# Performance work log

Hardware: AMD Instinct MI355X
Metric: run time of the kernel (lower is better)

## Reference

```python
import jax, jax.numpy as jnp
import numpy as np

LSTM_SIZE = 64
NUM_OPS = 5
NUM_LAYERS = 7  # 2 warmup anchors + 5 sampled layers (layer_id 2..6)


def _lstm_cell(x, h, c, w_ih, w_hh, b_ih, b_hh):
    # torch LSTMCell gate order: i, f, g, o
    g = x @ w_ih.T + b_ih + h @ w_hh.T + b_hh  # [1, 4*64]
    i, f, gg, o = jnp.split(g, 4, axis=1)
    c2 = jax.nn.sigmoid(f) * c + jax.nn.sigmoid(i) * jnp.tanh(gg)
    h2 = jax.nn.sigmoid(o) * jnp.tanh(c2)
    return h2, c2


def _sampler(embed, w_ih, w_hh, b_ih, b_hh, w_soft, b_soft, b_soft_no_learn,
             w_attn1, w_attn2, v_attn, prev_c, prev_h, use_bias, key):
    keys = jax.random.split(key, 20)  # 5 layers * (2 index + 2 op) samples
    k = 0
    anchors, anchors_w1, arc_seq = [], [], []
    log_prob = jnp.float32(0.0)
    entropy = jnp.float32(0.0)
    inputs = embed[0][None, :]
    # warmup: two anchor slots (anchors are zeros, per original code)
    for _ in range(2):
        prev_h, prev_c = _lstm_cell(inputs, prev_h, prev_c, w_ih, w_hh, b_ih, b_hh)
        anchors.append(jnp.zeros((1, LSTM_SIZE), jnp.float32))
        anchors_w1.append(prev_h @ w_attn1.T)
    for layer_id in range(2, NUM_LAYERS):
        idxs, ops = [], []
        # sample 2 previous-layer indices via tiny attention
        for _ in range(2):
            prev_h, prev_c = _lstm_cell(inputs, prev_h, prev_c, w_ih, w_hh, b_ih, b_hh)
            query = jnp.concatenate(anchors_w1, axis=0)            # [layer_id, 64]
            q = jnp.tanh(query + prev_h @ w_attn2.T)               # broadcast [layer_id, 64]
            logits = (q @ v_attn.T).reshape(layer_id)              # [layer_id]
            logits = logits / 5.0 + 1.1 * jnp.tanh(logits)
            index = jax.random.categorical(keys[k], logits); k += 1
            logp = jax.nn.log_softmax(logits)
            log_prob = log_prob + (-logp[index])
            entropy = entropy + jax.lax.stop_gradient(-jnp.sum(logp * jnp.exp(logp)))
            idxs.append(index)
            A = jnp.concatenate(anchors, axis=0)                   # [layer_id, 64]
            inputs = A[index][None, :]
        # sample 2 ops
        for _ in range(2):
            prev_h, prev_c = _lstm_cell(inputs, prev_h, prev_c, w_ih, w_hh, b_ih, b_hh)
            logits = (prev_h @ w_soft.T + b_soft)                  # [1, 5]
            logits = 1.1 / 2.5 * jnp.tanh(logits / 5.0)
            if use_bias:
                logits = logits + b_soft_no_learn
            logits = logits[0]
            op_id = jax.random.categorical(keys[k], logits); k += 1
            logp = jax.nn.log_softmax(logits)
            log_prob = log_prob + (-logp[op_id])
            entropy = entropy + jax.lax.stop_gradient(-jnp.sum(logp * jnp.exp(logp)))
            ops.append(op_id)
            inputs = embed[op_id + 1][None, :]
        # extra step producing this layer's anchor
        prev_h, prev_c = _lstm_cell(inputs, prev_h, prev_c, w_ih, w_hh, b_ih, b_hh)
        anchors.append(prev_h)
        anchors_w1.append(prev_h @ w_attn1.T)
        inputs = embed[0][None, :]
        # arc layout per layer after in-place fixups: [idx1, op1, idx2, op2]
        arc_seq += [idxs[0], ops[0], idxs[1], ops[1]]
    arc = jnp.stack(arc_seq)
    return arc, entropy, log_prob, prev_c, prev_h


def setup_inputs() -> dict:
    key = jax.random.key(0)
    ks = jax.random.split(key, 9)
    u = lambda k, shape: jax.random.uniform(k, shape, jnp.float32, -0.1, 0.1)
    return {
        "embed": u(ks[0], (6, LSTM_SIZE)),
        "w_ih": u(ks[1], (4 * LSTM_SIZE, LSTM_SIZE)),
        "w_hh": u(ks[2], (4 * LSTM_SIZE, LSTM_SIZE)),
        "b_ih": u(ks[3], (4 * LSTM_SIZE,)),
        "b_hh": u(ks[4], (4 * LSTM_SIZE,)),
        "w_soft": u(ks[5], (NUM_OPS, LSTM_SIZE)),
        "b_soft": jnp.array([[10.0, 10.0, 0.0, 0.0, 0.0]], jnp.float32),
        "b_soft_no_learn": jnp.array([[0.25, 0.25, -0.25, -0.25, -0.25]], jnp.float32),
        "w_attn1": u(ks[6], (LSTM_SIZE, LSTM_SIZE)),
        "w_attn2": u(ks[7], (LSTM_SIZE, LSTM_SIZE)),
        "v_attn": u(ks[8], (1, LSTM_SIZE)),
        "seed": 0,
    }


def reference(embed, w_ih, w_hh, b_ih, b_hh, w_soft, b_soft, b_soft_no_learn,
              w_attn1, w_attn2, v_attn, seed):
    key = jax.random.key(seed)
    k1, k2 = jax.random.split(key)
    zc = jnp.zeros((1, LSTM_SIZE), jnp.float32)
    zh = jnp.zeros((1, LSTM_SIZE), jnp.float32)
    arc1, ent1, lp1, c, h = _sampler(embed, w_ih, w_hh, b_ih, b_hh, w_soft, b_soft,
                                     b_soft_no_learn, w_attn1, w_attn2, v_attn,
                                     zc, zh, True, k1)
    arc2, ent2, lp2, _, _ = _sampler(embed, w_ih, w_hh, b_ih, b_hh, w_soft, b_soft,
                                     b_soft_no_learn, w_attn1, w_attn2, v_attn,
                                     c, h, False, k2)
    return (arc1, arc2, lp1 + lp2, ent1 + ent2)
```

## Files before the change

kernel.cpp:

```cpp
#include <hip/hip_runtime.h>
#include <cstdint>

#ifndef FASTMATH
#define FASTMATH 1
#endif

#define NT 512

__device__ __forceinline__ uint32_t rotl32_(uint32_t v, int d) {
  return (v << d) | (v >> (32 - d));
}

__device__ __forceinline__ void tf2x32(uint32_t k0, uint32_t k1,
                                       uint32_t x0, uint32_t x1,
                                       uint32_t& o0, uint32_t& o1) {
  const uint32_t k2 = k0 ^ k1 ^ 0x1BD11BDAu;
  x0 += k0; x1 += k1;
#define TF4(a,b,c,d) \
  x0 += x1; x1 = rotl32_(x1,a); x1 ^= x0; \
  x0 += x1; x1 = rotl32_(x1,b); x1 ^= x0; \
  x0 += x1; x1 = rotl32_(x1,c); x1 ^= x0; \
  x0 += x1; x1 = rotl32_(x1,d); x1 ^= x0;
  TF4(13,15,26,6)
  x0 += k1; x1 += k2 + 1u;
  TF4(17,29,16,24)
  x0 += k2; x1 += k0 + 2u;
  TF4(13,15,26,6)
  x0 += k0; x1 += k1 + 3u;
  TF4(17,29,16,24)
  x0 += k1; x1 += k2 + 4u;
  TF4(13,15,26,6)
  x0 += k2; x1 += k0 + 5u;
#undef TF4
  o0 = x0; o1 = x1;
}

#if FASTMATH
__device__ __forceinline__ float tanh_(float x) {
  float e = __expf(2.0f * x);
  return 1.0f - __fdividef(2.0f, e + 1.0f);
}
__device__ __forceinline__ float sig_(float x) {
  return __fdividef(1.0f, 1.0f + __expf(-x));
}
#define log_ __logf
#define exp_ __expf
#else
__device__ __forceinline__ float tanh_(float x) { return tanhf(x); }
__device__ __forceinline__ float sig_(float x) { return 0.5f * tanhf(0.5f * x) + 0.5f; }
#define log_ logf
#define exp_ expf
#endif

template <int CTRL>
__device__ __forceinline__ float dppf(float x) {
  return __int_as_float(__builtin_amdgcn_update_dpp(
      0, __float_as_int(x), CTRL, 0xF, 0xF, true));
}
template <int CTRL>
__device__ __forceinline__ int dppi(int x) {
  return __builtin_amdgcn_update_dpp(0, x, CTRL, 0xF, 0xF, true);
}
constexpr int QP1 = 0xB1;
constexpr int QP2 = 0x4E;
constexpr int HM  = 0x141;

__global__ __launch_bounds__(NT, 1)
void nas_controller(const float* __restrict__ embed,
                    const float* __restrict__ w_ih,
                    const float* __restrict__ w_hh,
                    const float* __restrict__ b_ih,
                    const float* __restrict__ b_hh,
                    const float* __restrict__ w_soft,
                    const float* __restrict__ b_soft,
                    const float* __restrict__ b_soft_nl,
                    const float* __restrict__ w_attn1,
                    const float* __restrict__ w_attn2,
                    const float* __restrict__ v_attn,
                    const int* __restrict__ seedp,
                    float* __restrict__ out) {
  const int tid  = threadIdx.x;
  const int lane = tid & 63;
  const int wid  = tid >> 6;
  const int row  = tid >> 1;
  const int half = tid & 1;

  __shared__ __align__(16) float attn1L[64 * 68];
  __shared__ __align__(16) float attn2L[64 * 68];
  __shared__ __align__(16) float wsoftL[5 * 68 + 8];
  __shared__ __align__(16) float vaL[64];
  __shared__ __align__(16) float preQ[13 * 256];
  __shared__ __align__(16) float aw1sL[8 * 68];
  __shared__ __align__(16) float hw2L[64];
  __shared__ __align__(16) float hB[64];
  __shared__ float cs[64];
  __shared__ float gates[256];
  __shared__ float gL[320];
  __shared__ float bsoftL[8], bnlL[8];
  __shared__ int   seliL;

  float4 wi[8], wh[8];
  {
    const float4* a = reinterpret_cast<const float4*>(w_ih) + row * 16 + half * 8;
#pragma unroll
    for (int j = 0; j < 8; ++j) wi[j] = a[j];
    const float4* b = reinterpret_cast<const float4*>(w_hh) + row * 16 + half * 8;
#pragma unroll
    for (int j = 0; j < 8; ++j) wh[j] = b[j];
  }
  const float bsum = b_ih[row] + b_hh[row];

  for (int i4 = tid; i4 < 1024; i4 += NT) {
    int r = i4 >> 4, c4 = i4 & 15;
    reinterpret_cast<float4*>(attn1L)[r * 17 + c4] =
        reinterpret_cast<const float4*>(w_attn1)[i4];
    reinterpret_cast<float4*>(attn2L)[r * 17 + c4] =
        reinterpret_cast<const float4*>(w_attn2)[i4];
  }
  for (int i = tid; i < 340; i += NT) {
    int r = i / 68, c = i % 68;
    wsoftL[i] = (c < 64) ? w_soft[r * 64 + c] : 0.f;
  }
  if (tid < 64) { vaL[tid] = v_attn[tid]; hB[tid] = 0.f; cs[tid] = 0.f; }
  if (tid < 8) {
    bsoftL[tid] = (tid < 5) ? b_soft[tid] : 0.f;
    bnlL[tid]   = (tid < 5) ? b_soft_nl[tid] : 0.f;
  }
  preQ[6 * 256 + tid] = 0.f;

  if (tid < 320) {
    int s_ = (tid >= 160) ? 1 : 0;
    int rem = tid - s_ * 160;
    int k = rem >> 3, i = rem & 7;
    uint32_t a, b, ka, kb, o0, o1;
    tf2x32(0u, (uint32_t)seedp[0], 0u, (uint32_t)s_, a, b);
    tf2x32(a, b, 0u, (uint32_t)k, ka, kb);
    tf2x32(ka, kb, 0u, (uint32_t)i, o0, o1);
    uint32_t bits = o0 ^ o1;
    const float TINY = 1.1754943508222875e-38f;
    float uu = __uint_as_float((bits >> 9) | 0x3f800000u) - 1.0f;
    uu = uu * (1.0f - TINY) + TINY;
    uu = fmaxf(TINY, uu);
    gL[tid] = -log_(-log_(uu));
  }

#pragma unroll
  for (int e = 0; e < 6; ++e) {
    const float4* x4 = reinterpret_cast<const float4*>(embed + e * 64) + half * 8;
    float a0 = 0, a1 = 0, a2 = 0, a3 = 0;
#pragma unroll
    for (int j = 0; j < 8; ++j) {
      float4 x = x4[j], w = wi[j];
      a0 = fmaf(w.x, x.x, a0); a1 = fmaf(w.y, x.y, a1);
      a2 = fmaf(w.z, x.z, a2); a3 = fmaf(w.w, x.w, a3);
    }
    float acc = (a0 + a1) + (a2 + a3);
    acc += __shfl_xor(acc, 1);
    if (half == 0) preQ[e * 256 + row] = acc;
  }

  __syncthreads();

  const float4* hU = reinterpret_cast<const float4*>(hB);
  float lp = 0.f, ent = 0.f;
  int srcSlot = 0, sIdx = 0;

  auto lstm = [&]() {
    const float4* h4 = reinterpret_cast<const float4*>(hB) + half * 8;
    float a0 = 0, a1 = 0, a2 = 0, a3 = 0;
#pragma unroll
    for (int j = 0; j < 8; ++j) {
      float4 x = h4[j], w = wh[j];
      a0 = fmaf(w.x, x.x, a0); a1 = fmaf(w.y, x.y, a1);
      a2 = fmaf(w.z, x.z, a2); a3 = fmaf(w.w, x.w, a3);
    }
    float acc = (a0 + a1) + (a2 + a3);
    acc += __shfl_xor(acc, 1);
    if (half == 0) gates[row] = acc + preQ[srcSlot * 256 + row] + bsum;
    __syncthreads();
    if (tid < 64) {
      float gi = gates[tid], gf = gates[64 + tid];
      float gg = gates[128 + tid], go = gates[192 + tid];
      float c2 = sig_(gf) * cs[tid] + sig_(gi) * tanh_(gg);
      float h2 = sig_(go) * tanh_(c2);
      cs[tid] = c2; hB[tid] = h2;
    }
  };

  auto matvecAll = [&](const float* W, float* dst) {
    const int r8 = tid >> 3, q = tid & 7;
    const float4* w4 = reinterpret_cast<const float4*>(W + r8 * 68 + q * 8);
    float4 wa = w4[0], wb = w4[1];
    const float4* h4 = reinterpret_cast<const float4*>(hB) + q * 2;
    float4 ha = h4[0], hb = h4[1];
    float acc = fmaf(wa.x, ha.x, fmaf(wa.y, ha.y, fmaf(wa.z, ha.z, wa.w * ha.w)));
    acc += fmaf(wb.x, hb.x, fmaf(wb.y, hb.y, fmaf(wb.z, hb.z, wb.w * hb.w)));
    acc += __shfl_xor(acc, 1);
    acc += __shfl_xor(acc, 2);
    acc += __shfl_xor(acc, 4);
    if (q == 0) dst[r8] = acc;
  };

  auto anchorPre = [&](int slot) {
    const float4* h4 = reinterpret_cast<const float4*>(hB) + half * 8;
    float a0 = 0, a1 = 0, a2 = 0, a3 = 0;
#pragma unroll
    for (int j = 0; j < 8; ++j) {
      float4 x = h4[j], w = wi[j];
      a0 = fmaf(w.x, x.x, a0); a1 = fmaf(w.y, x.y, a1);
      a2 = fmaf(w.z, x.z, a2); a3 = fmaf(w.w, x.w, a3);
    }
    float acc = (a0 + a1) + (a2 + a3);
    acc += __shfl_xor(acc, 1);
    if (half == 0) preQ[slot * 256 + row] = acc;
  };

  auto doSample = [&](int n, int k, int mode, float raw, float* op) {
    float l;
    if (lane < n) {
      if (mode == 0) l = raw / 5.0f + 1.1f * tanh_(raw);
      else {
        l = (float)(1.1 / 2.5) * tanh_(raw / 5.0f);
        if (mode == 1) l += bnlL[lane];
      }
    } else l = -INFINITY;
    float g = (lane < n) ? gL[sIdx * 160 + k * 8 + lane] : 0.f;
    float v = (lane < n) ? (l + g) : -INFINITY;
    int bi = lane & 7;
    float lw = l;
#define ARGSTEP(C) { float ov = dppf<C>(v), ol = dppf<C>(lw); int oi = dppi<C>(bi); \
    bool tk = (ov > v) || (ov == v && oi < bi); if (tk) { v = ov; lw = ol; bi = oi; } }
    ARGSTEP(QP1) ARGSTEP(QP2) ARGSTEP(HM)
#undef ARGSTEP
    float mx = l;
    mx = fmaxf(mx, dppf<QP1>(mx)); mx = fmaxf(mx, dppf<QP2>(mx)); mx = fmaxf(mx, dppf<HM>(mx));
    float e = (lane < n) ? exp_(l - mx) : 0.f;
    float ss = e; ss += dppf<QP1>(ss); ss += dppf<QP2>(ss); ss += dppf<HM>(ss);
    float lse = log_(ss);
    float lpi = l - mx - lse;
    float ec = (lane < n) ? lpi * exp_(lpi) : 0.f;
    ec += dppf<QP1>(ec); ec += dppf<QP2>(ec); ec += dppf<HM>(ec);
    if (lane == 0) {
      lp  += -(lw - mx - lse);
      ent += -ec;
      seliL = bi;
      op[0] = (float)bi;
    }
  };

  for (int s = 0; s < 2; ++s) {
    sIdx = s;
    srcSlot = 0;
    for (int w = 0; w < 2; ++w) {
      lstm();
      __syncthreads();
      matvecAll(attn1L, aw1sL + w * 68);
    }
    int keyk = 0;
    for (int L = 2; L <= 6; ++L) {
      for (int t = 0; t < 2; ++t) {
        lstm();
        __syncthreads();
        matvecAll(attn2L, hw2L);
        __syncthreads();
        if (wid == 0) {
          const int g8 = lane >> 3, j = lane & 7;
          float sacc = 0.f;
          if (g8 < L) {
            const float4* aw = reinterpret_cast<const float4*>(aw1sL + g8 * 68 + j * 8);
            const float4* hq = reinterpret_cast<const float4*>(hw2L + j * 8);
            const float4* vq = reinterpret_cast<const float4*>(vaL + j * 8);
            float4 A0 = aw[0], A1 = aw[1], H0 = hq[0], H1 = hq[1], V0 = vq[0], V1 = vq[1];
            sacc = fmaf(tanh_(A0.x + H0.x), V0.x, sacc);
            sacc = fmaf(tanh_(A0.y + H0.y), V0.y, sacc);
            sacc = fmaf(tanh_(A0.z + H0.z), V0.z, sacc);
            sacc = fmaf(tanh_(A0.w + H0.w), V0.w, sacc);
            sacc = fmaf(tanh_(A1.x + H1.x), V1.x, sacc);
            sacc = fmaf(tanh_(A1.y + H1.y), V1.y, sacc);
            sacc = fmaf(tanh_(A1.z + H1.z), V1.z, sacc);
            sacc = fmaf(tanh_(A1.w + H1.w), V1.w, sacc);
          }
          sacc += dppf<QP1>(sacc); sacc += dppf<QP2>(sacc); sacc += dppf<HM>(sacc);
          float raw = __shfl(sacc, lane << 3);
          doSample(L, keyk, 0, raw, out + s * 20 + (L - 2) * 4 + t * 2);
        }
        keyk++;
        __syncthreads();
        srcSlot = 6 + seliL;
      }
      for (int t = 0; t < 2; ++t) {
        lstm();
        if (wid == 0) {
          const int g8 = lane >> 3, j = lane & 7;
          float sacc = 0.f;
          if (g8 < 5) {
            const float4* wq = reinterpret_cast<const float4*>(wsoftL + g8 * 68 + j * 8);
            float4 wa = wq[0], wb = wq[1];
            float4 ha = hU[j * 2], hb = hU[j * 2 + 1];
            sacc = fmaf(wa.x, ha.x, fmaf(wa.y, ha.y, fmaf(wa.z, ha.z, wa.w * ha.w)));
            sacc += fmaf(wb.x, hb.x, fmaf(wb.y, hb.y, fmaf(wb.z, hb.z, wb.w * hb.w)));
          }
          sacc += dppf<QP1>(sacc); sacc += dppf<QP2>(sacc); sacc += dppf<HM>(sacc);
          float raw = __shfl(sacc, lane << 3) + bsoftL[lane & 7];
          doSample(5, keyk, (s == 0) ? 1 : 2, raw,
                   out + s * 20 + (L - 2) * 4 + t * 2 + 1);
        }
        keyk++;
        __syncthreads();
        srcSlot = 1 + seliL;
      }
      lstm();
      __syncthreads();
      matvecAll(attn1L, aw1sL + L * 68);
      anchorPre(6 + L);
      srcSlot = 0;
    }
  }

  if (tid == 0) { out[40] = lp; out[41] = ent; }
}

extern "C" void kernel_launch(void* const* d_in, const int* in_sizes, int n_in,
                              void* d_out, int out_size, void* d_ws, size_t ws_size,
                              hipStream_t stream) {
  (void)in_sizes; (void)n_in; (void)out_size; (void)d_ws; (void)ws_size;
  nas_controller<<<1, NT, 0, stream>>>(
      (const float*)d_in[0],
      (const float*)d_in[1],
      (const float*)d_in[2],
      (const float*)d_in[3],
      (const float*)d_in[4],
      (const float*)d_in[5],
      (const float*)d_in[6],
      (const float*)d_in[7],
      (const float*)d_in[8],
      (const float*)d_in[9],
      (const float*)d_in[10],
      (const int*)d_in[11],
      (float*)d_out);
}
```

Baseline: 74.70 us.

## Replicate LSTM nonlinearity and sampling per wave to cut barriers

Each wave now computes the LSTM gate nonlinearity and the categorical sampling redundantly. The cell state stays in a register and the selected index comes from readfirstlane rather than shared memory. Gates are double-buffered, so each recurrent step needs about one block barrier instead of several. This trades duplicated ALU and transcendental work across the eight waves, plus benign same-value writes to shared memory, for a shorter serial latency chain.

```diff
diff --git a/kernel.cpp b/kernel.cpp
--- a/kernel.cpp
+++ b/kernel.cpp
@@ -81,7 +81,6 @@
                     float* __restrict__ out) {
   const int tid  = threadIdx.x;
   const int lane = tid & 63;
-  const int wid  = tid >> 6;
   const int row  = tid >> 1;
   const int half = tid & 1;
 
@@ -93,11 +92,9 @@
   __shared__ __align__(16) float aw1sL[8 * 68];
   __shared__ __align__(16) float hw2L[64];
   __shared__ __align__(16) float hB[64];
-  __shared__ float cs[64];
-  __shared__ float gates[256];
+  __shared__ float gates[2][256];
   __shared__ float gL[320];
   __shared__ float bsoftL[8], bnlL[8];
-  __shared__ int   seliL;
 
   float4 wi[8], wh[8];
   {
@@ -121,7 +118,7 @@
     int r = i / 68, c = i % 68;
     wsoftL[i] = (c < 64) ? w_soft[r * 64 + c] : 0.f;
   }
-  if (tid < 64) { vaL[tid] = v_attn[tid]; hB[tid] = 0.f; cs[tid] = 0.f; }
+  if (tid < 64) { vaL[tid] = v_attn[tid]; hB[tid] = 0.f; }
   if (tid < 8) {
     bsoftL[tid] = (tid < 5) ? b_soft[tid] : 0.f;
     bnlL[tid]   = (tid < 5) ? b_soft_nl[tid] : 0.f;
@@ -161,11 +158,24 @@
 
   __syncthreads();
 
+  if (half == 0) gates[0][row] = preQ[0 * 256 + row] + bsum;
+  __syncthreads();
+
   const float4* hU = reinterpret_cast<const float4*>(hB);
+  float creg = 0.f;
   float lp = 0.f, ent = 0.f;
-  int srcSlot = 0, sIdx = 0;
-
-  auto lstm = [&]() {
+  int gp = 0, sIdx = 0;
+
+  auto nonlin = [&]() {
+    float gi = gates[gp][lane], gf = gates[gp][64 + lane];
+    float gg = gates[gp][128 + lane], go = gates[gp][192 + lane];
+    float c2 = sig_(gf) * creg + sig_(gi) * tanh_(gg);
+    float h2 = sig_(go) * tanh_(c2);
+    creg = c2;
+    hB[lane] = h2;
+  };
+
+  auto hdot = [&](int slot) {
     const float4* h4 = reinterpret_cast<const float4*>(hB) + half * 8;
     float a0 = 0, a1 = 0, a2 = 0, a3 = 0;
 #pragma unroll
@@ -176,15 +186,7 @@
     }
     float acc = (a0 + a1) + (a2 + a3);
     acc += __shfl_xor(acc, 1);
-    if (half == 0) gates[row] = acc + preQ[srcSlot * 256 + row] + bsum;
-    __syncthreads();
-    if (tid < 64) {
-      float gi = gates[tid], gf = gates[64 + tid];
-      float gg = gates[128 + tid], go = gates[192 + tid];
-      float c2 = sig_(gf) * cs[tid] + sig_(gi) * tanh_(gg);
-      float h2 = sig_(go) * tanh_(c2);
-      cs[tid] = c2; hB[tid] = h2;
-    }
+    if (half == 0) gates[gp ^ 1][row] = acc + preQ[slot * 256 + row] + bsum;
   };
 
   auto matvecAll = [&](const float* W, float* dst) {
@@ -215,7 +217,7 @@
     if (half == 0) preQ[slot * 256 + row] = acc;
   };
 
-  auto doSample = [&](int n, int k, int mode, float raw, float* op) {
+  auto doSampleR = [&](int n, int k, int mode, float raw, float* op) -> int {
     float l;
     if (lane < n) {
       if (mode == 0) l = raw / 5.0f + 1.1f * tanh_(raw);
@@ -243,77 +245,72 @@
     if (lane == 0) {
       lp  += -(lw - mx - lse);
       ent += -ec;
-      seliL = bi;
-      op[0] = (float)bi;
-    }
+      if (tid == 0) op[0] = (float)bi;
+    }
+    return __builtin_amdgcn_readfirstlane(bi);
   };
 
   for (int s = 0; s < 2; ++s) {
     sIdx = s;
-    srcSlot = 0;
     for (int w = 0; w < 2; ++w) {
-      lstm();
-      __syncthreads();
+      nonlin();
       matvecAll(attn1L, aw1sL + w * 68);
+      hdot(0);
+      __syncthreads(); gp ^= 1;
     }
     int keyk = 0;
     for (int L = 2; L <= 6; ++L) {
       for (int t = 0; t < 2; ++t) {
-        lstm();
-        __syncthreads();
+        nonlin();
         matvecAll(attn2L, hw2L);
         __syncthreads();
-        if (wid == 0) {
-          const int g8 = lane >> 3, j = lane & 7;
-          float sacc = 0.f;
-          if (g8 < L) {
-            const float4* aw = reinterpret_cast<const float4*>(aw1sL + g8 * 68 + j * 8);
-            const float4* hq = reinterpret_cast<const float4*>(hw2L + j * 8);
-            const float4* vq = reinterpret_cast<const float4*>(vaL + j * 8);
-            float4 A0 = aw[0], A1 = aw[1], H0 = hq[0], H1 = hq[1], V0 = vq[0], V1 = vq[1];
-            sacc = fmaf(tanh_(A0.x + H0.x), V0.x, sacc);
-            sacc = fmaf(tanh_(A0.y + H0.y), V0.y, sacc);
-            sacc = fmaf(tanh_(A0.z + H0.z), V0.z, sacc);
-            sacc = fmaf(tanh_(A0.w + H0.w), V0.w, sacc);
-            sacc = fmaf(tanh_(A1.x + H1.x), V1.x, sacc);
-            sacc = fmaf(tanh_(A1.y + H1.y), V1.y, sacc);
-            sacc = fmaf(tanh_(A1.z + H1.z), V1.z, sacc);
-            sacc = fmaf(tanh_(A1.w + H1.w), V1.w, sacc);
-          }
-          sacc += dppf<QP1>(sacc); sacc += dppf<QP2>(sacc); sacc += dppf<HM>(sacc);
-          float raw = __shfl(sacc, lane << 3);
-          doSample(L, keyk, 0, raw, out + s * 20 + (L - 2) * 4 + t * 2);
+        const int g8 = lane >> 3, j = lane & 7;
+        float sacc = 0.f;
+        if (g8 < L) {
+          const float4* aw = reinterpret_cast<const float4*>(aw1sL + g8 * 68 + j * 8);
+          const float4* hq = reinterpret_cast<const float4*>(hw2L + j * 8);
+          const float4* vq = reinterpret_cast<const float4*>(vaL + j * 8);
+          float4 A0 = aw[0], A1 = aw[1], H0 = hq[0], H1 = hq[1], V0 = vq[0], V1 = vq[1];
+          sacc = fmaf(tanh_(A0.x + H0.x), V0.x, sacc);
+          sacc = fmaf(tanh_(A0.y + H0.y), V0.y, sacc);
+          sacc = fmaf(tanh_(A0.z + H0.z), V0.z, sacc);
+          sacc = fmaf(tanh_(A0.w + H0.w), V0.w, sacc);
+          sacc = fmaf(tanh_(A1.x + H1.x), V1.x, sacc);
+          sacc = fmaf(tanh_(A1.y + H1.y), V1.y, sacc);
+          sacc = fmaf(tanh_(A1.z + H1.z), V1.z, sacc);
+          sacc = fmaf(tanh_(A1.w + H1.w), V1.w, sacc);
         }
+        sacc += dppf<QP1>(sacc); sacc += dppf<QP2>(sacc); sacc += dppf<HM>(sacc);
+        float raw = __shfl(sacc, lane << 3);
+        int sel = doSampleR(L, keyk, 0, raw, out + s * 20 + (L - 2) * 4 + t * 2);
         keyk++;
-        __syncthreads();
-        srcSlot = 6 + seliL;
+        hdot(6 + sel);
+        __syncthreads(); gp ^= 1;
       }
       for (int t = 0; t < 2; ++t) {
-        lstm();
-        if (wid == 0) {
-          const int g8 = lane >> 3, j = lane & 7;
-          float sacc = 0.f;
-          if (g8 < 5) {
-            const float4* wq = reinterpret_cast<const float4*>(wsoftL + g8 * 68 + j * 8);
-            float4 wa = wq[0], wb = wq[1];
-            float4 ha = hU[j * 2], hb = hU[j * 2 + 1];
-            sacc = fmaf(wa.x, ha.x, fmaf(wa.y, ha.y, fmaf(wa.z, ha.z, wa.w * ha.w)));
-            sacc += fmaf(wb.x, hb.x, fmaf(wb.y, hb.y, fmaf(wb.z, hb.z, wb.w * hb.w)));
-          }
-          sacc += dppf<QP1>(sacc); sacc += dppf<QP2>(sacc); sacc += dppf<HM>(sacc);
-          float raw = __shfl(sacc, lane << 3) + bsoftL[lane & 7];
-          doSample(5, keyk, (s == 0) ? 1 : 2, raw,
-                   out + s * 20 + (L - 2) * 4 + t * 2 + 1);
+        nonlin();
+        const int g8 = lane >> 3, j = lane & 7;
+        float sacc = 0.f;
+        if (g8 < 5) {
+          const float4* wq = reinterpret_cast<const float4*>(wsoftL + g8 * 68 + j * 8);
+          float4 wa = wq[0], wb = wq[1];
+          float4 ha = hU[j * 2], hb = hU[j * 2 + 1];
+          sacc = fmaf(wa.x, ha.x, fmaf(wa.y, ha.y, fmaf(wa.z, ha.z, wa.w * ha.w)));
+          sacc += fmaf(wb.x, hb.x, fmaf(wb.y, hb.y, fmaf(wb.z, hb.z, wb.w * hb.w)));
         }
+        sacc += dppf<QP1>(sacc); sacc += dppf<QP2>(sacc); sacc += dppf<HM>(sacc);
+        float raw = __shfl(sacc, lane << 3) + bsoftL[lane & 7];
+        int sel = doSampleR(5, keyk, (s == 0) ? 1 : 2, raw,
+                            out + s * 20 + (L - 2) * 4 + t * 2 + 1);
         keyk++;
-        __syncthreads();
-        srcSlot = 1 + seliL;
+        hdot(1 + sel);
+        __syncthreads(); gp ^= 1;
       }
-      lstm();
-      __syncthreads();
+      nonlin();
       matvecAll(attn1L, aw1sL + L * 68);
       anchorPre(6 + L);
-      srcSlot = 0;
+      hdot(0);
+      __syncthreads(); gp ^= 1;
     }
   }
 
```

Result: slower. 90.24 us (+20.8%).

## Defer log-softmax/entropy to a parallel epilogue and precompute h·W_hh early

Applied to the files above, without the earlier changes.

Each sampling step now only computes the logits and the Gumbel argmax. The logits and selected indices are saved to shared memory, and a final parallel pass over 320 threads computes log-prob and entropy. The recurrent h·W_hh dot product is hoisted to run right after the nonlinearity, alongside the attention matvec, so the next step only adds preQ and bias before its barrier. This takes the softmax reductions and several transcendentals off the serial critical path, at the cost of extra barriers and a small epilogue.

```diff
diff --git a/kernel.cpp b/kernel.cpp
--- a/kernel.cpp
+++ b/kernel.cpp
@@ -96,6 +96,9 @@
   __shared__ float cs[64];
   __shared__ float gates[256];
   __shared__ float gL[320];
+  __shared__ float lSave[320];
+  __shared__ float lpT[40], entT[40];
+  __shared__ int   biSave[40];
   __shared__ float bsoftL[8], bnlL[8];
   __shared__ int   seliL;
 
@@ -162,22 +165,10 @@
   __syncthreads();
 
   const float4* hU = reinterpret_cast<const float4*>(hB);
-  float lp = 0.f, ent = 0.f;
+  float hacc = 0.f;
   int srcSlot = 0, sIdx = 0;
 
-  auto lstm = [&]() {
-    const float4* h4 = reinterpret_cast<const float4*>(hB) + half * 8;
-    float a0 = 0, a1 = 0, a2 = 0, a3 = 0;
-#pragma unroll
-    for (int j = 0; j < 8; ++j) {
-      float4 x = h4[j], w = wh[j];
-      a0 = fmaf(w.x, x.x, a0); a1 = fmaf(w.y, x.y, a1);
-      a2 = fmaf(w.z, x.z, a2); a3 = fmaf(w.w, x.w, a3);
-    }
-    float acc = (a0 + a1) + (a2 + a3);
-    acc += __shfl_xor(acc, 1);
-    if (half == 0) gates[row] = acc + preQ[srcSlot * 256 + row] + bsum;
-    __syncthreads();
+  auto nonlin = [&]() {
     if (tid < 64) {
       float gi = gates[tid], gf = gates[64 + tid];
       float gg = gates[128 + tid], go = gates[192 + tid];
@@ -185,6 +176,20 @@
       float h2 = sig_(go) * tanh_(c2);
       cs[tid] = c2; hB[tid] = h2;
     }
+  };
+
+  auto hdotAcc = [&]() -> float {
+    const float4* h4 = reinterpret_cast<const float4*>(hB) + half * 8;
+    float a0 = 0, a1 = 0, a2 = 0, a3 = 0;
+#pragma unroll
+    for (int j = 0; j < 8; ++j) {
+      float4 x = h4[j], w = wh[j];
+      a0 = fmaf(w.x, x.x, a0); a1 = fmaf(w.y, x.y, a1);
+      a2 = fmaf(w.z, x.z, a2); a3 = fmaf(w.w, x.w, a3);
+    }
+    float acc = (a0 + a1) + (a2 + a3);
+    acc += __shfl_xor(acc, 1);
+    return acc;
   };
 
   auto matvecAll = [&](const float* W, float* dst) {
@@ -215,7 +220,7 @@
     if (half == 0) preQ[slot * 256 + row] = acc;
   };
 
-  auto doSample = [&](int n, int k, int mode, float raw, float* op) {
+  auto doSel = [&](int n, int k, int mode, float raw, float* op) {
     float l;
     if (lane < n) {
       if (mode == 0) l = raw / 5.0f + 1.1f * tanh_(raw);
@@ -224,26 +229,17 @@
         if (mode == 1) l += bnlL[lane];
       }
     } else l = -INFINITY;
+    if (lane < 8) lSave[(sIdx * 20 + k) * 8 + lane] = l;
     float g = (lane < n) ? gL[sIdx * 160 + k * 8 + lane] : 0.f;
     float v = (lane < n) ? (l + g) : -INFINITY;
     int bi = lane & 7;
-    float lw = l;
-#define ARGSTEP(C) { float ov = dppf<C>(v), ol = dppf<C>(lw); int oi = dppi<C>(bi); \
-    bool tk = (ov > v) || (ov == v && oi < bi); if (tk) { v = ov; lw = ol; bi = oi; } }
+#define ARGSTEP(C) { float ov = dppf<C>(v); int oi = dppi<C>(bi); \
+    bool tk = (ov > v) || (ov == v && oi < bi); if (tk) { v = ov; bi = oi; } }
     ARGSTEP(QP1) ARGSTEP(QP2) ARGSTEP(HM)
 #undef ARGSTEP
-    float mx = l;
-    mx = fmaxf(mx, dppf<QP1>(mx)); mx = fmaxf(mx, dppf<QP2>(mx)); mx = fmaxf(mx, dppf<HM>(mx));
-    float e = (lane < n) ? exp_(l - mx) : 0.f;
-    float ss = e; ss += dppf<QP1>(ss); ss += dppf<QP2>(ss); ss += dppf<HM>(ss);
-    float lse = log_(ss);
-    float lpi = l - mx - lse;
-    float ec = (lane < n) ? lpi * exp_(lpi) : 0.f;
-    ec += dppf<QP1>(ec); ec += dppf<QP2>(ec); ec += dppf<HM>(ec);
     if (lane == 0) {
-      lp  += -(lw - mx - lse);
-      ent += -ec;
       seliL = bi;
+      biSave[sIdx * 20 + k] = bi;
       op[0] = (float)bi;
     }
   };
@@ -252,15 +248,22 @@
     sIdx = s;
     srcSlot = 0;
     for (int w = 0; w < 2; ++w) {
-      lstm();
-      __syncthreads();
+      if (half == 0) gates[row] = hacc + preQ[srcSlot * 256 + row] + bsum;
+      __syncthreads();
+      nonlin();
+      __syncthreads();
+      hacc = hdotAcc();
       matvecAll(attn1L, aw1sL + w * 68);
+      __syncthreads();
     }
     int keyk = 0;
     for (int L = 2; L <= 6; ++L) {
       for (int t = 0; t < 2; ++t) {
-        lstm();
-        __syncthreads();
+        if (half == 0) gates[row] = hacc + preQ[srcSlot * 256 + row] + bsum;
+        __syncthreads();
+        nonlin();
+        __syncthreads();
+        hacc = hdotAcc();
         matvecAll(attn2L, hw2L);
         __syncthreads();
         if (wid == 0) {
@@ -282,14 +285,18 @@
           }
           sacc += dppf<QP1>(sacc); sacc += dppf<QP2>(sacc); sacc += dppf<HM>(sacc);
           float raw = __shfl(sacc, lane << 3);
-          doSample(L, keyk, 0, raw, out + s * 20 + (L - 2) * 4 + t * 2);
+          doSel(L, keyk, 0, raw, out + s * 20 + (L - 2) * 4 + t * 2);
         }
         keyk++;
         __syncthreads();
         srcSlot = 6 + seliL;
       }
       for (int t = 0; t < 2; ++t) {
-        lstm();
+        if (half == 0) gates[row] = hacc + preQ[srcSlot * 256 + row] + bsum;
+        __syncthreads();
+        nonlin();
+        __syncthreads();
+        hacc = hdotAcc();
         if (wid == 0) {
           const int g8 = lane >> 3, j = lane & 7;
           float sacc = 0.f;
@@ -302,22 +309,46 @@
           }
           sacc += dppf<QP1>(sacc); sacc += dppf<QP2>(sacc); sacc += dppf<HM>(sacc);
           float raw = __shfl(sacc, lane << 3) + bsoftL[lane & 7];
-          doSample(5, keyk, (s == 0) ? 1 : 2, raw,
-                   out + s * 20 + (L - 2) * 4 + t * 2 + 1);
+          doSel(5, keyk, (s == 0) ? 1 : 2, raw,
+                out + s * 20 + (L - 2) * 4 + t * 2 + 1);
         }
         keyk++;
         __syncthreads();
         srcSlot = 1 + seliL;
       }
-      lstm();
-      __syncthreads();
+      if (half == 0) gates[row] = hacc + preQ[srcSlot * 256 + row] + bsum;
+      __syncthreads();
+      nonlin();
+      __syncthreads();
+      hacc = hdotAcc();
       matvecAll(attn1L, aw1sL + L * 68);
       anchorPre(6 + L);
+      __syncthreads();
       srcSlot = 0;
     }
   }
 
-  if (tid == 0) { out[40] = lp; out[41] = ent; }
+  __syncthreads();
+  if (tid < 320) {
+    int j = tid >> 3, c = tid & 7;
+    float l = lSave[j * 8 + c];
+    float mx = l;
+    mx = fmaxf(mx, dppf<QP1>(mx)); mx = fmaxf(mx, dppf<QP2>(mx)); mx = fmaxf(mx, dppf<HM>(mx));
+    float e = (l == -INFINITY) ? 0.f : exp_(l - mx);
+    float ss = e; ss += dppf<QP1>(ss); ss += dppf<QP2>(ss); ss += dppf<HM>(ss);
+    float lse = log_(ss);
+    float lpi = l - mx - lse;
+    float ec = (l == -INFINITY) ? 0.f : lpi * exp_(lpi);
+    ec += dppf<QP1>(ec); ec += dppf<QP2>(ec); ec += dppf<HM>(ec);
+    if (c == 0) entT[j] = -ec;
+    if (c == biSave[j]) lpT[j] = -(l - mx - lse);
+  }
+  __syncthreads();
+  if (tid == 0) {
+    float lp = 0.f, ent = 0.f;
+    for (int j = 0; j < 40; ++j) { lp += lpT[j]; ent += entT[j]; }
+    out[40] = lp; out[41] = ent;
+  }
 }
 
 extern "C" void kernel_launch(void* const* d_in, const int* in_sizes, int n_in,
```

Result: faster. 72.72 us (-2.7%).
